# Kernel tuning notes

Measured on AMD Instinct MI355X. Metric: run time of the kernel, lower is better.

The kernel has to match this reference:

```python
import jax, jax.numpy as jnp
import numpy as np

D_HEAD = 64  # per-head dim 'd' from init_kwargs


def layer_norm(x, g, b, eps=1e-5):
    m = x.mean(-1, keepdims=True)
    v = x.var(-1, keepdims=True)  # biased var, matches torch LayerNorm
    return (x - m) / jnp.sqrt(v + eps) * g + b


def setup_inputs() -> dict:
    key = jax.random.key(0)
    ks = jax.random.split(key, 16)
    F = 512
    B, T, N = 2, 8, 1024
    s = 1.0 / np.sqrt(F)
    u = lambda k, shape: jax.random.uniform(k, shape, jnp.float32, -s, s)
    return {
        "x": jax.random.normal(ks[0], (B, T, N, F), jnp.float32),
        "Wq": u(ks[1], (F, F)), "bq": u(ks[2], (F,)),
        "Wk": u(ks[3], (F, F)), "bk": u(ks[4], (F,)),
        "Wv": u(ks[5], (F, F)), "bv": u(ks[6], (F,)),
        "ln_g": jnp.ones((F,), jnp.float32), "ln_b": jnp.zeros((F,), jnp.float32),
        "W1": u(ks[7], (F, F)), "b1": u(ks[8], (F,)),
        "W2": u(ks[9], (F, F)), "b2": u(ks[10], (F,)),
        "lnff_g": jnp.ones((F,), jnp.float32), "lnff_b": jnp.zeros((F,), jnp.float32),
    }


def reference(x, Wq, bq, Wk, bk, Wv, bv, ln_g, ln_b, W1, b1, W2, b2, lnff_g, lnff_b):
    B, T, N, F = x.shape
    h = F // D_HEAD
    # q/k/v projections
    q = x @ Wq + bq
    k = x @ Wk + bk
    v = x @ Wv + bv
    # split last dim into heads (split+cat(dim=0) in torch == head axis here)
    qh = q.reshape(B, T, N, h, D_HEAD)
    kh = k.reshape(B, T, N, h, D_HEAD)
    vh = v.reshape(B, T, N, h, D_HEAD)
    # attention over node axis N per (batch, time, head)
    A = jnp.einsum('btqhd,btkhd->bthqk', qh, kh) / jnp.sqrt(jnp.asarray(D_HEAD, x.dtype))
    A = jax.nn.softmax(A, axis=-1)
    o = jnp.einsum('bthqk,btkhd->btqhd', A, vh).reshape(B, T, N, F)
    # residual + LN
    val = layer_norm(o + x, ln_g, ln_b)
    # FFN + final LN
    ff = jax.nn.relu(val @ W1 + b1) @ W2 + b2
    return layer_norm(ff, lnff_g, lnff_b)
```

## Files before the change

### kernel.cpp

```cpp
#include <hip/hip_runtime.h>
#include <hip/hip_bf16.h>

using bf16 = __hip_bfloat16;
typedef unsigned int u32x4 __attribute__((ext_vector_type(4)));
typedef float f32x4 __attribute__((ext_vector_type(4)));
typedef __bf16 bf16x8 __attribute__((ext_vector_type(8)));

#define DEVI __device__ __forceinline__

DEVI f32x4 mfma16(u32x4 a, u32x4 b, f32x4 c) {
    return __builtin_amdgcn_mfma_f32_16x16x32_bf16(
        __builtin_bit_cast(bf16x8, a), __builtin_bit_cast(bf16x8, b), c, 0, 0, 0);
}

struct bf8 { bf16 h[8]; };

DEVI u32x4 pack8(f32x4 lo, f32x4 hi) {
    bf8 t;
#pragma unroll
    for (int i = 0; i < 4; i++) {
        t.h[i] = __float2bfloat16(lo[i]);
        t.h[4 + i] = __float2bfloat16(hi[i]);
    }
    return __builtin_bit_cast(u32x4, t);
}

DEVI void async16(const bf16* g, bf16* l) {
    __builtin_amdgcn_global_load_lds(
        (const __attribute__((address_space(1))) unsigned int*)g,
        (__attribute__((address_space(3))) unsigned int*)l, 16, 0, 0);
}

__global__ __launch_bounds__(256) void prep_weights(
    const float* __restrict__ Wq, const float* __restrict__ Wk,
    const float* __restrict__ Wv, const float* __restrict__ W1,
    const float* __restrict__ W2, bf16* __restrict__ WT)
{
    int w = blockIdx.y;
    const float* src = (w == 0) ? Wq : (w == 1) ? Wk : (w == 2) ? Wv : (w == 3) ? W1 : W2;
    int idx = blockIdx.x * 256 + threadIdx.x;
    int n = idx >> 9, kk = idx & 511;
    WT[(size_t)w * 262144 + idx] = __float2bfloat16(src[kk * 512 + n]);
}

__global__ __launch_bounds__(256) void prep_x(const float* __restrict__ x, bf16* __restrict__ xb)
{
    size_t i = ((size_t)blockIdx.x * 256 + threadIdx.x) * 8;
    f32x4 lo = *(const f32x4*)&x[i];
    f32x4 hi = *(const f32x4*)&x[i + 4];
    *(u32x4*)&xb[i] = pack8(lo, hi);
}

enum { EPI_NONE = 0, EPI_RELU = 1, EPI_VT = 2, EPI_SCALE = 3 };

template <int EPI>
__global__ __launch_bounds__(256) void gemm_bt(
    const bf16* __restrict__ A, const bf16* __restrict__ Bt,
    const float* __restrict__ bias, bf16* __restrict__ C)
{
    __shared__ __align__(16) bf16 As[128 * 32];
    __shared__ __align__(16) bf16 Bs[128 * 32];
    const int tid = threadIdx.x;
    const int lane = tid & 63, wave = tid >> 6;
    const int wm = (wave >> 1) * 64, wn = (wave & 1) * 64;
    const int bm = blockIdx.x * 128, bn = blockIdx.y * 128;
    const int lm = lane & 15, lq = lane >> 4;

    f32x4 acc[4][4];
#pragma unroll
    for (int i = 0; i < 4; i++)
#pragma unroll
        for (int j = 0; j < 4; j++) acc[i][j] = (f32x4){0.f, 0.f, 0.f, 0.f};

    for (int k0 = 0; k0 < 512; k0 += 32) {
        __syncthreads();
#pragma unroll
        for (int p = 0; p < 2; p++) {
            int c = p * 256 + tid;
            int r = c >> 2, kc = (c & 3) * 8;
            async16(&A[(size_t)(bm + r) * 512 + k0 + kc], &As[(p * 256 + wave * 64) * 8]);
            async16(&Bt[(size_t)(bn + r) * 512 + k0 + kc], &Bs[(p * 256 + wave * 64) * 8]);
        }
        __syncthreads();
        u32x4 af[4], bfr[4];
#pragma unroll
        for (int i = 0; i < 4; i++) af[i] = *(const u32x4*)&As[(wm + i * 16 + lm) * 32 + lq * 8];
#pragma unroll
        for (int j = 0; j < 4; j++) bfr[j] = *(const u32x4*)&Bs[(wn + j * 16 + lm) * 32 + lq * 8];
#pragma unroll
        for (int i = 0; i < 4; i++)
#pragma unroll
            for (int j = 0; j < 4; j++) acc[i][j] = mfma16(af[i], bfr[j], acc[i][j]);
    }

#pragma unroll
    for (int i = 0; i < 4; i++) {
#pragma unroll
        for (int j = 0; j < 4; j++) {
            int col = bn + wn + j * 16 + lm;
            float bv = bias[col];
#pragma unroll
            for (int r = 0; r < 4; r++) {
                int row = bm + wm + i * 16 + lq * 4 + r;
                float cv = acc[i][j][r] + bv;
                if (EPI == EPI_RELU) cv = fmaxf(cv, 0.f);
                if (EPI == EPI_SCALE) cv *= 0.18033688f;
                if (EPI == EPI_VT) {
                    int bt = row >> 10, node = row & 1023;
                    int hh = col >> 6, d = col & 63;
                    C[((size_t)((bt * 8 + hh) * 64 + d)) * 1024 + node] = __float2bfloat16(cv);
                } else {
                    C[(size_t)row * 512 + col] = __float2bfloat16(cv);
                }
            }
        }
    }
}

__global__ __launch_bounds__(256) void attn_kernel(
    const bf16* __restrict__ q, const bf16* __restrict__ k,
    const bf16* __restrict__ vT, float* __restrict__ o)
{
    constexpr int KP = 72;
    constexpr int VP = 80;
    __shared__ __align__(16) bf16 Ks[64 * KP];
    __shared__ __align__(16) bf16 Vs[64 * VP];
    __shared__ __align__(16) bf16 Ps[4][32 * VP];

    const int tid = threadIdx.x, lane = tid & 63, wave = tid >> 6;
    const int group = blockIdx.y;
    const int bt = group >> 3, hh = group & 7;
    const int lm = lane & 15, lq = lane >> 4;
    const int qrow0 = bt * 1024 + blockIdx.x * 128 + wave * 32;

    u32x4 qf[2][2];
#pragma unroll
    for (int tm = 0; tm < 2; tm++)
#pragma unroll
        for (int kk = 0; kk < 2; kk++)
            qf[tm][kk] = *(const u32x4*)&q[(size_t)(qrow0 + tm * 16 + lm) * 512 + hh * 64 + kk * 32 + lq * 8];

    f32x4 accO[2][4];
#pragma unroll
    for (int tm = 0; tm < 2; tm++)
#pragma unroll
        for (int tn = 0; tn < 4; tn++) accO[tm][tn] = (f32x4){0.f, 0.f, 0.f, 0.f};
    float part[2] = {0.f, 0.f};

    for (int kt = 0; kt < 16; kt++) {
        __syncthreads();
#pragma unroll
        for (int p = 0; p < 2; p++) {
            int c = p * 256 + tid;
            int row = c >> 3, e8 = (c & 7) * 8;
            *(u32x4*)&Ks[row * KP + e8] =
                *(const u32x4*)&k[(size_t)(bt * 1024 + kt * 64 + row) * 512 + hh * 64 + e8];
            *(u32x4*)&Vs[row * VP + e8] =
                *(const u32x4*)&vT[(size_t)(group * 64 + row) * 1024 + kt * 64 + e8];
        }
        __syncthreads();

#pragma unroll
        for (int tk = 0; tk < 4; tk++) {
            u32x4 kf0 = *(const u32x4*)&Ks[(tk * 16 + lm) * KP + lq * 8];
            u32x4 kf1 = *(const u32x4*)&Ks[(tk * 16 + lm) * KP + 32 + lq * 8];
#pragma unroll
            for (int tm = 0; tm < 2; tm++) {
                f32x4 st = (f32x4){0.f, 0.f, 0.f, 0.f};
                st = mfma16(kf0, qf[tm][0], st);
                st = mfma16(kf1, qf[tm][1], st);
                float p0 = exp2f(st[0]), p1 = exp2f(st[1]);
                float p2 = exp2f(st[2]), p3 = exp2f(st[3]);
                part[tm] += (p0 + p1) + (p2 + p3);
                union { unsigned long long u; bf16 h[4]; } pk;
                pk.h[0] = __float2bfloat16(p0); pk.h[1] = __float2bfloat16(p1);
                pk.h[2] = __float2bfloat16(p2); pk.h[3] = __float2bfloat16(p3);
                *(unsigned long long*)&Ps[wave][(tm * 16 + lm) * VP + tk * 16 + lq * 4] = pk.u;
            }
        }

#pragma unroll
        for (int kc = 0; kc < 2; kc++) {
            u32x4 pf[2], vf[4];
#pragma unroll
            for (int tm = 0; tm < 2; tm++)
                pf[tm] = *(const u32x4*)&Ps[wave][(tm * 16 + lm) * VP + kc * 32 + lq * 8];
#pragma unroll
            for (int tn = 0; tn < 4; tn++)
                vf[tn] = *(const u32x4*)&Vs[(tn * 16 + lm) * VP + kc * 32 + lq * 8];
#pragma unroll
            for (int tm = 0; tm < 2; tm++)
#pragma unroll
                for (int tn = 0; tn < 4; tn++)
                    accO[tm][tn] = mfma16(pf[tm], vf[tn], accO[tm][tn]);
        }
    }

#pragma unroll
    for (int tm = 0; tm < 2; tm++) {
        part[tm] += __shfl_xor(part[tm], 16);
        part[tm] += __shfl_xor(part[tm], 32);
    }
#pragma unroll
    for (int tm = 0; tm < 2; tm++)
#pragma unroll
        for (int r = 0; r < 4; r++) {
            float l = __shfl(part[tm], lq * 4 + r);
            float linv = 1.0f / l;
#pragma unroll
            for (int tn = 0; tn < 4; tn++) {
                int row = qrow0 + tm * 16 + lq * 4 + r;
                int col = hh * 64 + tn * 16 + lm;
                o[(size_t)row * 512 + col] = accO[tm][tn][r] * linv;
            }
        }
}

template <bool AF32, bool RES, bool OF32>
__global__ __launch_bounds__(256) void ln_kernel(
    const void* __restrict__ a, const float* __restrict__ res,
    const float* __restrict__ g, const float* __restrict__ bb, void* __restrict__ out)
{
    int row = blockIdx.x * 4 + (threadIdx.x >> 6);
    int lane = threadIdx.x & 63;
    size_t base = (size_t)row * 512 + lane * 8;
    int cbase = lane * 8;

    float x8[8];
    if (AF32) {
        const float* af = (const float*)a;
        f32x4 lo = *(const f32x4*)&af[base];
        f32x4 hi = *(const f32x4*)&af[base + 4];
#pragma unroll
        for (int i = 0; i < 4; i++) { x8[i] = lo[i]; x8[4 + i] = hi[i]; }
    } else {
        bf8 av = __builtin_bit_cast(bf8, *(const u32x4*)&((const bf16*)a)[base]);
#pragma unroll
        for (int i = 0; i < 8; i++) x8[i] = __bfloat162float(av.h[i]);
    }
    if (RES) {
        f32x4 lo = *(const f32x4*)&res[base];
        f32x4 hi = *(const f32x4*)&res[base + 4];
#pragma unroll
        for (int i = 0; i < 4; i++) { x8[i] += lo[i]; x8[4 + i] += hi[i]; }
    }

    float s = 0.f, s2 = 0.f;
#pragma unroll
    for (int i = 0; i < 8; i++) { s += x8[i]; s2 += x8[i] * x8[i]; }
#pragma unroll
    for (int off = 1; off < 64; off <<= 1) {
        s += __shfl_xor(s, off);
        s2 += __shfl_xor(s2, off);
    }
    float mean = s * (1.f / 512.f);
    float var = s2 * (1.f / 512.f) - mean * mean;
    float rstd = rsqrtf(var + 1e-5f);

    f32x4 g0 = *(const f32x4*)&g[cbase], g1 = *(const f32x4*)&g[cbase + 4];
    f32x4 b0 = *(const f32x4*)&bb[cbase], b1v = *(const f32x4*)&bb[cbase + 4];
    float y[8];
#pragma unroll
    for (int i = 0; i < 4; i++) {
        y[i] = (x8[i] - mean) * rstd * g0[i] + b0[i];
        y[4 + i] = (x8[4 + i] - mean) * rstd * g1[i] + b1v[i];
    }
    if (OF32) {
        float* op = (float*)out;
        *(f32x4*)&op[base] = (f32x4){y[0], y[1], y[2], y[3]};
        *(f32x4*)&op[base + 4] = (f32x4){y[4], y[5], y[6], y[7]};
    } else {
        bf8 ov;
#pragma unroll
        for (int i = 0; i < 8; i++) ov.h[i] = __float2bfloat16(y[i]);
        *(u32x4*)&((bf16*)out)[base] = __builtin_bit_cast(u32x4, ov);
    }
}

extern "C" void kernel_launch(void* const* d_in, const int* in_sizes, int n_in,
                              void* d_out, int out_size, void* d_ws, size_t ws_size,
                              hipStream_t stream)
{
    const float* x    = (const float*)d_in[0];
    const float* Wq   = (const float*)d_in[1];
    const float* bq   = (const float*)d_in[2];
    const float* Wk   = (const float*)d_in[3];
    const float* bk   = (const float*)d_in[4];
    const float* Wv   = (const float*)d_in[5];
    const float* bv   = (const float*)d_in[6];
    const float* ln_g = (const float*)d_in[7];
    const float* ln_b = (const float*)d_in[8];
    const float* W1   = (const float*)d_in[9];
    const float* b1   = (const float*)d_in[10];
    const float* W2   = (const float*)d_in[11];
    const float* b2   = (const float*)d_in[12];
    const float* lnffg = (const float*)d_in[13];
    const float* lnffb = (const float*)d_in[14];
    float* out = (float*)d_out;

    bf16* ws = (bf16*)d_ws;
    bf16* WT = ws;
    bf16* qb = ws + 5 * 262144;
    bf16* kb = qb + 8388608;
    bf16* vT = kb + 8388608;
    bf16* vl = qb;
    bf16* f1 = kb;
    bf16* f2 = vT;
    bf16* xb = (bf16*)d_out;

    prep_weights<<<dim3(1024, 5), 256, 0, stream>>>(Wq, Wk, Wv, W1, W2, WT);
    prep_x<<<4096, 256, 0, stream>>>(x, xb);

    dim3 gg(128, 4);
    gemm_bt<EPI_SCALE><<<gg, 256, 0, stream>>>(xb, WT + 0 * 262144, bq, qb);
    gemm_bt<EPI_NONE> <<<gg, 256, 0, stream>>>(xb, WT + 1 * 262144, bk, kb);
    gemm_bt<EPI_VT>   <<<gg, 256, 0, stream>>>(xb, WT + 2 * 262144, bv, vT);

    attn_kernel<<<dim3(8, 128), 256, 0, stream>>>(qb, kb, vT, out);

    ln_kernel<true, true, false><<<4096, 256, 0, stream>>>(out, x, ln_g, ln_b, vl);

    gemm_bt<EPI_RELU><<<gg, 256, 0, stream>>>(vl, WT + 3 * 262144, b1, f1);
    gemm_bt<EPI_NONE><<<gg, 256, 0, stream>>>(f1, WT + 4 * 262144, b2, f2);

    ln_kernel<false, false, true><<<4096, 256, 0, stream>>>(f2, nullptr, lnffg, lnffb, out);
}
```

Baseline: 288.2 us.

## Merge QKV GEMMs into one launch and cheapen attention exp and bf16 packing

```diff
diff --git a/kernel.cpp b/kernel.cpp
--- a/kernel.cpp
+++ b/kernel.cpp
@@ -23,6 +23,14 @@
         t.h[4 + i] = __float2bfloat16(hi[i]);
     }
     return __builtin_bit_cast(u32x4, t);
+}
+
+DEVI unsigned rne2(float a, float b) {
+    unsigned ua = __builtin_bit_cast(unsigned, a);
+    unsigned ub = __builtin_bit_cast(unsigned, b);
+    ua += 0x7FFFu + ((ua >> 16) & 1u);
+    ub += 0x7FFFu + ((ub >> 16) & 1u);
+    return __builtin_amdgcn_perm(ub, ua, 0x07060302);
 }
 
 DEVI void async16(const bf16* g, bf16* l) {
@@ -51,9 +59,75 @@
     *(u32x4*)&xb[i] = pack8(lo, hi);
 }
 
-enum { EPI_NONE = 0, EPI_RELU = 1, EPI_VT = 2, EPI_SCALE = 3 };
-
-template <int EPI>
+
+__global__ __launch_bounds__(256) void gemm_qkv(
+    const bf16* __restrict__ A, const bf16* __restrict__ WT,
+    const float* __restrict__ bqp, const float* __restrict__ bkp, const float* __restrict__ bvp,
+    bf16* __restrict__ qb, bf16* __restrict__ kb, bf16* __restrict__ vT)
+{
+    __shared__ __align__(16) bf16 As[128 * 32];
+    __shared__ __align__(16) bf16 Bs[128 * 32];
+    const int tid = threadIdx.x;
+    const int lane = tid & 63, wave = tid >> 6;
+    const int wm = (wave >> 1) * 64, wn = (wave & 1) * 64;
+    const int wsel = blockIdx.y >> 2;
+    const int bm = blockIdx.x * 128, bn = (blockIdx.y & 3) * 128;
+    const bf16* Bt = WT + (size_t)wsel * 262144;
+    const float* bias = (wsel == 0) ? bqp : (wsel == 1) ? bkp : bvp;
+    const int lm = lane & 15, lq = lane >> 4;
+
+    f32x4 acc[4][4];
+#pragma unroll
+    for (int i = 0; i < 4; i++)
+#pragma unroll
+        for (int j = 0; j < 4; j++) acc[i][j] = (f32x4){0.f, 0.f, 0.f, 0.f};
+
+    for (int k0 = 0; k0 < 512; k0 += 32) {
+        __syncthreads();
+#pragma unroll
+        for (int p = 0; p < 2; p++) {
+            int c = p * 256 + tid;
+            int r = c >> 2, kc = (c & 3) * 8;
+            async16(&A[(size_t)(bm + r) * 512 + k0 + kc], &As[(p * 256 + wave * 64) * 8]);
+            async16(&Bt[(size_t)(bn + r) * 512 + k0 + kc], &Bs[(p * 256 + wave * 64) * 8]);
+        }
+        __syncthreads();
+        u32x4 af[4], bfr[4];
+#pragma unroll
+        for (int i = 0; i < 4; i++) af[i] = *(const u32x4*)&As[(wm + i * 16 + lm) * 32 + lq * 8];
+#pragma unroll
+        for (int j = 0; j < 4; j++) bfr[j] = *(const u32x4*)&Bs[(wn + j * 16 + lm) * 32 + lq * 8];
+#pragma unroll
+        for (int i = 0; i < 4; i++)
+#pragma unroll
+            for (int j = 0; j < 4; j++) acc[i][j] = mfma16(af[i], bfr[j], acc[i][j]);
+    }
+
+#pragma unroll
+    for (int i = 0; i < 4; i++) {
+#pragma unroll
+        for (int j = 0; j < 4; j++) {
+            int col = bn + wn + j * 16 + lm;
+            float bv = bias[col];
+#pragma unroll
+            for (int r = 0; r < 4; r++) {
+                int row = bm + wm + i * 16 + lq * 4 + r;
+                float cv = acc[i][j][r] + bv;
+                if (wsel == 0) {
+                    qb[(size_t)row * 512 + col] = __float2bfloat16(cv * 0.18033688f);
+                } else if (wsel == 1) {
+                    kb[(size_t)row * 512 + col] = __float2bfloat16(cv);
+                } else {
+                    int bt = row >> 10, node = row & 1023;
+                    int hh = col >> 6, d = col & 63;
+                    vT[((size_t)((bt * 8 + hh) * 64 + d)) * 1024 + node] = __float2bfloat16(cv);
+                }
+            }
+        }
+    }
+}
+
+template <bool RELU>
 __global__ __launch_bounds__(256) void gemm_bt(
     const bf16* __restrict__ A, const bf16* __restrict__ Bt,
     const float* __restrict__ bias, bf16* __restrict__ C)
@@ -103,15 +177,8 @@
             for (int r = 0; r < 4; r++) {
                 int row = bm + wm + i * 16 + lq * 4 + r;
                 float cv = acc[i][j][r] + bv;
-                if (EPI == EPI_RELU) cv = fmaxf(cv, 0.f);
-                if (EPI == EPI_SCALE) cv *= 0.18033688f;
-                if (EPI == EPI_VT) {
-                    int bt = row >> 10, node = row & 1023;
-                    int hh = col >> 6, d = col & 63;
-                    C[((size_t)((bt * 8 + hh) * 64 + d)) * 1024 + node] = __float2bfloat16(cv);
-                } else {
-                    C[(size_t)row * 512 + col] = __float2bfloat16(cv);
-                }
+                if (RELU) cv = fmaxf(cv, 0.f);
+                C[(size_t)row * 512 + col] = __float2bfloat16(cv);
             }
         }
     }
@@ -122,7 +189,7 @@
     const bf16* __restrict__ vT, float* __restrict__ o)
 {
     constexpr int KP = 72;
-    constexpr int VP = 80;
+    constexpr int VP = 72;
     __shared__ __align__(16) bf16 Ks[64 * KP];
     __shared__ __align__(16) bf16 Vs[64 * VP];
     __shared__ __align__(16) bf16 Ps[4][32 * VP];
@@ -169,13 +236,14 @@
                 f32x4 st = (f32x4){0.f, 0.f, 0.f, 0.f};
                 st = mfma16(kf0, qf[tm][0], st);
                 st = mfma16(kf1, qf[tm][1], st);
-                float p0 = exp2f(st[0]), p1 = exp2f(st[1]);
-                float p2 = exp2f(st[2]), p3 = exp2f(st[3]);
+                float p0 = __builtin_amdgcn_exp2f(st[0]);
+                float p1 = __builtin_amdgcn_exp2f(st[1]);
+                float p2 = __builtin_amdgcn_exp2f(st[2]);
+                float p3 = __builtin_amdgcn_exp2f(st[3]);
                 part[tm] += (p0 + p1) + (p2 + p3);
-                union { unsigned long long u; bf16 h[4]; } pk;
-                pk.h[0] = __float2bfloat16(p0); pk.h[1] = __float2bfloat16(p1);
-                pk.h[2] = __float2bfloat16(p2); pk.h[3] = __float2bfloat16(p3);
-                *(unsigned long long*)&Ps[wave][(tm * 16 + lm) * VP + tk * 16 + lq * 4] = pk.u;
+                unsigned lo = rne2(p0, p1), hi = rne2(p2, p3);
+                unsigned long long pk = ((unsigned long long)hi << 32) | lo;
+                *(unsigned long long*)&Ps[wave][(tm * 16 + lm) * VP + tk * 16 + lq * 4] = pk;
             }
         }
 
@@ -311,17 +379,15 @@
     prep_weights<<<dim3(1024, 5), 256, 0, stream>>>(Wq, Wk, Wv, W1, W2, WT);
     prep_x<<<4096, 256, 0, stream>>>(x, xb);
 
+    gemm_qkv<<<dim3(128, 12), 256, 0, stream>>>(xb, WT, bq, bk, bv, qb, kb, vT);
+
+    attn_kernel<<<dim3(8, 128), 256, 0, stream>>>(qb, kb, vT, out);
+
+    ln_kernel<true, true, false><<<4096, 256, 0, stream>>>(out, x, ln_g, ln_b, vl);
+
     dim3 gg(128, 4);
-    gemm_bt<EPI_SCALE><<<gg, 256, 0, stream>>>(xb, WT + 0 * 262144, bq, qb);
-    gemm_bt<EPI_NONE> <<<gg, 256, 0, stream>>>(xb, WT + 1 * 262144, bk, kb);
-    gemm_bt<EPI_VT>   <<<gg, 256, 0, stream>>>(xb, WT + 2 * 262144, bv, vT);
-
-    attn_kernel<<<dim3(8, 128), 256, 0, stream>>>(qb, kb, vT, out);
-
-    ln_kernel<true, true, false><<<4096, 256, 0, stream>>>(out, x, ln_g, ln_b, vl);
-
-    gemm_bt<EPI_RELU><<<gg, 256, 0, stream>>>(vl, WT + 3 * 262144, b1, f1);
-    gemm_bt<EPI_NONE><<<gg, 256, 0, stream>>>(f1, WT + 4 * 262144, b2, f2);
+    gemm_bt<true> <<<gg, 256, 0, stream>>>(vl, WT + 3 * 262144, b1, f1);
+    gemm_bt<false><<<gg, 256, 0, stream>>>(f1, WT + 4 * 262144, b2, f2);
 
     ln_kernel<false, false, true><<<4096, 256, 0, stream>>>(f2, nullptr, lnffg, lnffb, out);
 }
```

After: 278.5 us. -3.4%, faster.
